# Optimization experiments

Measured on AMD Instinct MI355X. Metric: run time of the kernel, lower is better.

Reference implementation:

```python
import jax, jax.numpy as jnp
import numpy as np

MAX_DISTANCE = 50.0
NUM_BINS = 50
FEATURE_DIM = 64
B, K = 2048, 1024


def setup_inputs() -> dict:
    key = jax.random.key(0)
    k1, k2, k3, k4, k5, k6 = jax.random.split(key, 6)
    goal_positions = jax.random.normal(k1, (B, K, 2), dtype=jnp.float32) * 20.0
    ego_state = jax.random.normal(k2, (B, 4), dtype=jnp.float32)
    in_dim = NUM_BINS + 6  # 56
    s1 = 1.0 / np.sqrt(in_dim)
    s2 = 1.0 / np.sqrt(FEATURE_DIM)
    W1 = jax.random.uniform(k3, (in_dim, FEATURE_DIM), jnp.float32, -s1, s1)
    b1 = jax.random.uniform(k4, (FEATURE_DIM,), jnp.float32, -s1, s1)
    W2 = jax.random.uniform(k5, (FEATURE_DIM, 1), jnp.float32, -s2, s2)
    b2 = jax.random.uniform(k6, (1,), jnp.float32, -s2, s2)
    return {"goal_positions": goal_positions, "ego_state": ego_state,
            "W1": W1, "b1": b1, "W2": W2, "b2": b2}


def _histogram(goal_positions):
    # distances: (B, K); bin_idx = min(int(d / max_d * num_bins), num_bins - 1)
    d = jnp.linalg.norm(goal_positions, axis=-1)
    idx = jnp.floor(d / MAX_DISTANCE * NUM_BINS).astype(jnp.int32)
    idx = jnp.clip(idx, 0, NUM_BINS - 1)
    return jax.nn.one_hot(idx, NUM_BINS, dtype=goal_positions.dtype)  # (B, K, num_bins)


def reference(goal_positions, ego_state, W1, b1, W2, b2):
    hist = _histogram(goal_positions)                              # (B, K, nb)
    ego = jnp.broadcast_to(ego_state[:, None, :],
                           (goal_positions.shape[0], goal_positions.shape[1], 4))
    feats = jnp.concatenate([hist, goal_positions, ego], axis=-1)  # (B, K, nb+6)
    h = jax.nn.relu(jnp.einsum('bkf,fd->bkd', feats, W1) + b1)     # (B, K, feature_dim)
    scores = (jnp.einsum('bkd,do->bko', h, W2) + b2)[..., 0]       # (B, K)
    return scores
```

## Files before the change

kernel.cpp:

```cpp
#include <hip/hip_runtime.h>

#define NBIN 50
#define DIM  64
#define TPB  256

typedef _Float16 h2 __attribute__((ext_vector_type(2)));

__device__ __forceinline__ h2 u32_h2(unsigned int u) {
    union { unsigned int u; h2 h; } c; c.u = u; return c.h;
}
__device__ __forceinline__ unsigned int h2_u32(h2 h) {
    union { h2 h; unsigned int u; } c; c.h = h; return c.u;
}

template <int CTRL>
__device__ __forceinline__ float dpp_add(float v) {
    int m = __builtin_amdgcn_mov_dpp(__float_as_int(v), CTRL, 0xF, 0xF, true);
    return v + __int_as_float(m);
}

__global__ __launch_bounds__(TPB, 8) void scorer_kernel(
    const float* __restrict__ goal,
    const float* __restrict__ ego,
    const float* __restrict__ W1,
    const float* __restrict__ b1,
    const float* __restrict__ W2,
    const float* __restrict__ b2,
    float* __restrict__ out)
{
    __shared__ uint4 comb[NBIN * 8];
    __shared__ uint2 sxy[1024];

    const int b    = blockIdx.x;
    const int tid  = threadIdx.x;
    const int lane = tid & 63;
    const int w    = tid >> 6;

    const float4 eg = ((const float4*)ego)[b];
    const int   dp = tid & 31;
    const int   d0 = dp * 2, d1 = d0 + 1;
    const float ev0 = b1[d0] + eg.x * W1[52*DIM+d0] + eg.y * W1[53*DIM+d0]
                             + eg.z * W1[54*DIM+d0] + eg.w * W1[55*DIM+d0];
    const float ev1 = b1[d1] + eg.x * W1[52*DIM+d1] + eg.y * W1[53*DIM+d1]
                             + eg.z * W1[54*DIM+d1] + eg.w * W1[55*DIM+d1];
    for (int pi = tid; pi < NBIN * 32; pi += TPB) {
        int bin = pi >> 5;
        float2 wv = ((const float2*)W1)[bin * 32 + dp];
        h2 hv = {(_Float16)(wv.x + ev0), (_Float16)(wv.y + ev1)};
        ((unsigned int*)comb)[bin * 32 + dp] = h2_u32(hv);
    }

    const float2* gp = (const float2*)goal + (size_t)b * 1024 + w * 256;
#pragma unroll
    for (int r = 0; r < 4; ++r) {
        float2 pv = gp[r * 64 + lane];
        float r2 = __fadd_rn(__fmul_rn(pv.x, pv.x), __fmul_rn(pv.y, pv.y));
        float fv = floorf(__fmul_rn(__fdiv_rn(__fsqrt_rn(r2), 50.0f), 50.0f));
        int ix = (int)fv;
        ix = ix < 0 ? 0 : (ix > NBIN - 1 ? NBIN - 1 : ix);
        h2 xyh = {(_Float16)pv.x, (_Float16)pv.y};
        sxy[w * 256 + r * 64 + lane] = make_uint2(h2_u32(xyh), (unsigned)(ix * 8));
    }
    __syncthreads();

    const int dd = (lane & 7) * 8;
    const float4 al = *(const float4*)(W1 + 50 * DIM + dd);
    const float4 ah = *(const float4*)(W1 + 50 * DIM + dd + 4);
    const float4 ul = *(const float4*)(W1 + 51 * DIM + dd);
    const float4 uh = *(const float4*)(W1 + 51 * DIM + dd + 4);
    const float4 cl = *(const float4*)(W2 + dd);
    const float4 ch = *(const float4*)(W2 + dd + 4);
    const h2 wa0 = {(_Float16)al.x, (_Float16)al.y}, wa1 = {(_Float16)al.z, (_Float16)al.w};
    const h2 wa2 = {(_Float16)ah.x, (_Float16)ah.y}, wa3 = {(_Float16)ah.z, (_Float16)ah.w};
    const h2 wu0 = {(_Float16)ul.x, (_Float16)ul.y}, wu1 = {(_Float16)ul.z, (_Float16)ul.w};
    const h2 wu2 = {(_Float16)uh.x, (_Float16)uh.y}, wu3 = {(_Float16)uh.z, (_Float16)uh.w};
    const h2 wc0 = {(_Float16)cl.x, (_Float16)cl.y}, wc1 = {(_Float16)cl.z, (_Float16)cl.w};
    const h2 wc2 = {(_Float16)ch.x, (_Float16)ch.y}, wc3 = {(_Float16)ch.z, (_Float16)ch.w};
    const h2 hz = {(_Float16)0.0f, (_Float16)0.0f};
    const float bias2 = b2[0];

    const int   sel   = lane & 7;
    const int   ebase = w * 256 + (lane >> 3) * 8;
    const uint4* gpt  = comb + (lane & 7);

#define PAIR(GW, WA, WU, WC)                                                  \
    {                                                                         \
        h2 gg = u32_h2(GW);                                                   \
        h2 tt;                                                                \
        asm("v_pk_fma_f16 %0, %1, %2, %3 op_sel:[1,0,0] op_sel_hi:[1,1,1]"    \
            : "=v"(tt) : "v"(xy), "v"(WU), "v"(gg));                          \
        asm("v_pk_fma_f16 %0, %1, %2, %0 op_sel:[0,0,0] op_sel_hi:[0,1,1]"    \
            : "+v"(tt) : "v"(xy), "v"(WA));                                   \
        asm("v_pk_max_f16 %0, %0, %1" : "+v"(tt) : "v"(hz));                  \
        acc = __builtin_amdgcn_fdot2(tt, WC, acc, false);                     \
    }

#pragma unroll
    for (int r = 0; r < 4; ++r) {
        float keep = 0.0f;
#pragma unroll
        for (int s = 0; s < 8; ++s) {
            uint2 e  = sxy[ebase + r * 64 + s];
            h2    xy = u32_h2(e.x);
            uint4 gv = gpt[e.y];
            float acc = 0.0f;
            PAIR(gv.x, wa0, wu0, wc0);
            PAIR(gv.y, wa1, wu1, wc1);
            PAIR(gv.z, wa2, wu2, wc2);
            PAIR(gv.w, wa3, wu3, wc3);
            acc = dpp_add<0xB1>(acc);
            acc = dpp_add<0x4E>(acc);
            acc = dpp_add<0x141>(acc);
            keep = (s == sel) ? acc : keep;
        }
        out[(size_t)b * 1024 + w * 256 + r * 64 + lane] = keep + bias2;
    }
#undef PAIR
}

extern "C" void kernel_launch(void* const* d_in, const int* in_sizes, int n_in,
                              void* d_out, int out_size, void* d_ws, size_t ws_size,
                              hipStream_t stream) {
    const float* goal = (const float*)d_in[0];
    const float* ego  = (const float*)d_in[1];
    const float* W1   = (const float*)d_in[2];
    const float* b1   = (const float*)d_in[3];
    const float* W2   = (const float*)d_in[4];
    const float* b2   = (const float*)d_in[5];
    float* out = (float*)d_out;

    int B = in_sizes[1] / 4;
    scorer_kernel<<<dim3(B), dim3(TPB), 0, stream>>>(goal, ego, W1, b1, W2, b2, out);
}
```

Baseline: 21.90 us.

## Replace LDS point staging with swizzle broadcasts and transpose-style reduction

Each lane now keeps its point's fp16 xy and bin offset in registers instead of writing them to a shared array. The eight points of an octet are broadcast to the other lanes with ds_swizzle. The per-point 8-lane reduction, previously three DPP adds per point followed by a select, becomes a butterfly transpose-reduce: pairs of partial sums are exchanged with DPP and a swizzle, so each lane ends up with its own point's score. This cuts LDS traffic and the number of cross-lane ops per round, but adds swizzle instructions and selects, and may raise register pressure.

Result: no change. 21.66 us (-1.1%).

```diff
diff --git a/kernel.cpp b/kernel.cpp
--- a/kernel.cpp
+++ b/kernel.cpp
@@ -14,10 +14,14 @@
 }
 
 template <int CTRL>
-__device__ __forceinline__ float dpp_add(float v) {
-    int m = __builtin_amdgcn_mov_dpp(__float_as_int(v), CTRL, 0xF, 0xF, true);
-    return v + __int_as_float(m);
+__device__ __forceinline__ float xg_dpp(float v) {
+    return __int_as_float(__builtin_amdgcn_mov_dpp(__float_as_int(v), CTRL, 0xF, 0xF, true));
 }
+__device__ __forceinline__ float xg_sw4(float v) {
+    return __int_as_float(__builtin_amdgcn_ds_swizzle(__float_as_int(v), 0x101F));
+}
+
+#define SW_OCT(v, S) __builtin_amdgcn_ds_swizzle((v), (((S) << 5) | 0x18))
 
 __global__ __launch_bounds__(TPB, 8) void scorer_kernel(
     const float* __restrict__ goal,
@@ -29,12 +33,25 @@
     float* __restrict__ out)
 {
     __shared__ uint4 comb[NBIN * 8];
-    __shared__ uint2 sxy[1024];
 
     const int b    = blockIdx.x;
     const int tid  = threadIdx.x;
     const int lane = tid & 63;
     const int w    = tid >> 6;
+
+    const float2* gp = (const float2*)goal + (size_t)b * 1024 + w * 256;
+    int xyh[4], bo[4];
+#pragma unroll
+    for (int r = 0; r < 4; ++r) {
+        float2 pv = gp[r * 64 + lane];
+        float r2 = __fadd_rn(__fmul_rn(pv.x, pv.x), __fmul_rn(pv.y, pv.y));
+        float fv = floorf(__fmul_rn(__fdiv_rn(__fsqrt_rn(r2), 50.0f), 50.0f));
+        int ix = (int)fv;
+        ix = ix < 0 ? 0 : (ix > NBIN - 1 ? NBIN - 1 : ix);
+        bo[r] = ix * 8;
+        h2 xyp = {(_Float16)pv.x, (_Float16)pv.y};
+        xyh[r] = (int)h2_u32(xyp);
+    }
 
     const float4 eg = ((const float4*)ego)[b];
     const int   dp = tid & 31;
@@ -48,18 +65,6 @@
         float2 wv = ((const float2*)W1)[bin * 32 + dp];
         h2 hv = {(_Float16)(wv.x + ev0), (_Float16)(wv.y + ev1)};
         ((unsigned int*)comb)[bin * 32 + dp] = h2_u32(hv);
-    }
-
-    const float2* gp = (const float2*)goal + (size_t)b * 1024 + w * 256;
-#pragma unroll
-    for (int r = 0; r < 4; ++r) {
-        float2 pv = gp[r * 64 + lane];
-        float r2 = __fadd_rn(__fmul_rn(pv.x, pv.x), __fmul_rn(pv.y, pv.y));
-        float fv = floorf(__fmul_rn(__fdiv_rn(__fsqrt_rn(r2), 50.0f), 50.0f));
-        int ix = (int)fv;
-        ix = ix < 0 ? 0 : (ix > NBIN - 1 ? NBIN - 1 : ix);
-        h2 xyh = {(_Float16)pv.x, (_Float16)pv.y};
-        sxy[w * 256 + r * 64 + lane] = make_uint2(h2_u32(xyh), (unsigned)(ix * 8));
     }
     __syncthreads();
 
@@ -79,9 +84,8 @@
     const h2 hz = {(_Float16)0.0f, (_Float16)0.0f};
     const float bias2 = b2[0];
 
-    const int   sel   = lane & 7;
-    const int   ebase = w * 256 + (lane >> 3) * 8;
-    const uint4* gpt  = comb + (lane & 7);
+    const uint4* gpt = comb + (lane & 7);
+    const bool p1 = (lane & 1) != 0, p2 = (lane & 2) != 0, p4 = (lane & 4) != 0;
 
 #define PAIR(GW, WA, WU, WC)                                                  \
     {                                                                         \
@@ -95,26 +99,43 @@
         acc = __builtin_amdgcn_fdot2(tt, WC, acc, false);                     \
     }
 
-#pragma unroll
-    for (int r = 0; r < 4; ++r) {
-        float keep = 0.0f;
-#pragma unroll
-        for (int s = 0; s < 8; ++s) {
-            uint2 e  = sxy[ebase + r * 64 + s];
-            h2    xy = u32_h2(e.x);
-            uint4 gv = gpt[e.y];
-            float acc = 0.0f;
-            PAIR(gv.x, wa0, wu0, wc0);
-            PAIR(gv.y, wa1, wu1, wc1);
-            PAIR(gv.z, wa2, wu2, wc2);
-            PAIR(gv.w, wa3, wu3, wc3);
-            acc = dpp_add<0xB1>(acc);
-            acc = dpp_add<0x4E>(acc);
-            acc = dpp_add<0x141>(acc);
-            keep = (s == sel) ? acc : keep;
-        }
-        out[(size_t)b * 1024 + w * 256 + r * 64 + lane] = keep + bias2;
+#define S_ITER(S, ACC)                                                        \
+    {                                                                         \
+        h2   xy = u32_h2((unsigned)SW_OCT(xyr, S));                           \
+        int  bos = SW_OCT(bor, S);                                            \
+        uint4 gv = gpt[bos];                                                  \
+        float acc = 0.0f;                                                     \
+        PAIR(gv.x, wa0, wu0, wc0);                                            \
+        PAIR(gv.y, wa1, wu1, wc1);                                            \
+        PAIR(gv.z, wa2, wu2, wc2);                                            \
+        PAIR(gv.w, wa3, wu3, wc3);                                            \
+        ACC = acc;                                                            \
     }
+
+#define ROUND(R)                                                              \
+    {                                                                         \
+        const int xyr = xyh[R], bor = bo[R];                                  \
+        float a0, a1, a2, a3, a4, a5, a6, a7;                                 \
+        S_ITER(0, a0) S_ITER(1, a1) S_ITER(2, a2) S_ITER(3, a3)               \
+        S_ITER(4, a4) S_ITER(5, a5) S_ITER(6, a6) S_ITER(7, a7)               \
+               \
+        float q0 = (p1 ? a1 : a0) + xg_dpp<0xB1>(p1 ? a0 : a1);               \
+        float q1 = (p1 ? a3 : a2) + xg_dpp<0xB1>(p1 ? a2 : a3);               \
+        float q2 = (p1 ? a5 : a4) + xg_dpp<0xB1>(p1 ? a4 : a5);               \
+        float q3 = (p1 ? a7 : a6) + xg_dpp<0xB1>(p1 ? a6 : a7);               \
+        float r0 = (p2 ? q1 : q0) + xg_dpp<0x4E>(p2 ? q0 : q1);               \
+        float r1 = (p2 ? q3 : q2) + xg_dpp<0x4E>(p2 ? q2 : q3);               \
+        float vf = (p4 ? r1 : r0) + xg_sw4(p4 ? r0 : r1);                     \
+        out[(size_t)b * 1024 + w * 256 + (R) * 64 + lane] = vf + bias2;       \
+    }
+
+    ROUND(0)
+    ROUND(1)
+    ROUND(2)
+    ROUND(3)
+
+#undef ROUND
+#undef S_ITER
 #undef PAIR
 }
 
```
